# Performance work log

Hardware: AMD Instinct MI355X
Metric: run time of the kernel (lower is better)

## Reference

```python
import jax, jax.numpy as jnp
import numpy as np

DIM = 512; QS = 64; QT = 16; KS = 256; KT = 16; WIN = 4; B = 8; RANK = 32


def build_local_mask():
    # centers = round(linspace(0, kv_steps-1, q_steps)); valid kv step iff |s - center| <= window
    centers = np.round(np.linspace(0.0, KS - 1, QS)).astype(np.int64)
    s = np.arange(KS)
    valid = np.abs(s[None, :] - centers[:, None]) <= WIN  # [QS, KS]
    m = np.where(valid, 0.0, -np.inf).astype(np.float32)
    m = np.repeat(np.repeat(m, QT, axis=0), KT, axis=1)  # [QS*QT, KS*KT]
    return jnp.asarray(m)


def layer_norm(x, g, b, eps=1e-5):
    mu = jnp.mean(x, axis=-1, keepdims=True)
    var = jnp.mean((x - mu) ** 2, axis=-1, keepdims=True)
    return (x - mu) * jax.lax.rsqrt(var + eps) * g + b


def setup_inputs() -> dict:
    key = jax.random.key(0)
    ks = jax.random.split(key, 16)
    w = lambda k, shape: (jax.random.normal(k, shape, jnp.float32) * 0.02)
    return {
        'query': jax.random.normal(ks[0], (B, QS, QT, DIM), jnp.float32),
        'source': jax.random.normal(ks[1], (B, KS, KT, DIM), jnp.float32),
        'ctx0': jax.random.normal(ks[2], (B, DIM), jnp.float32),
        'ctx1': jax.random.normal(ks[3], (B, DIM), jnp.float32),
        'mask': build_local_mask(),
        'qn_g': jnp.ones(DIM), 'qn_b': jnp.zeros(DIM),
        'kvn_g': jnp.ones(DIM), 'kvn_b': jnp.zeros(DIM),
        'Wq': w(ks[4], (DIM, DIM)), 'bq': jnp.zeros(DIM),
        'Wk': w(ks[5], (DIM, DIM)), 'bk': jnp.zeros(DIM),
        'Wv': w(ks[6], (DIM, DIM)), 'bv': jnp.zeros(DIM),
        'Wo': w(ks[7], (DIM, DIM)), 'bo': jnp.zeros(DIM),
        'Wgq': w(ks[8], (DIM, RANK)),
        'Wgk': w(ks[9], (DIM, RANK)),
        'Wc0': w(ks[10], (DIM, DIM)), 'bc0': jnp.zeros(DIM),
        'Wc1': w(ks[11], (DIM, DIM)), 'bc1': jnp.zeros(DIM),
        'Wf': w(ks[12], (DIM, 2 * DIM)), 'bf': jnp.zeros(2 * DIM),
    }


def reference(query, source, ctx0, ctx1, mask, qn_g, qn_b, kvn_g, kvn_b,
              Wq, bq, Wk, bk, Wv, bv, Wo, bo, Wgq, Wgk,
              Wc0, bc0, Wc1, bc1, Wf, bf):
    b = query.shape[0]
    # MultiContextCondition: per-context linear, pooled, FiLM head -> (gamma, beta)
    h = jax.nn.silu(ctx0 @ Wc0 + bc0 + ctx1 @ Wc1 + bc1)          # [b, dim]
    gamma, beta = jnp.split(h @ Wf + bf, 2, axis=-1)              # [b, dim] each
    q_flat = query.reshape(b, QS * QT, DIM)
    s_flat = source.reshape(b, KS * KT, DIM)
    q_base = layer_norm(q_flat, qn_g, qn_b)
    s_base = layer_norm(s_flat, kvn_g, kvn_b)
    q_mod = q_base * (1.0 + gamma[:, None, :]) + beta[:, None, :]
    q_p = q_mod @ Wq + bq
    k_p = s_base @ Wk + bk
    v_p = s_base @ Wv + bv
    scale = DIM ** -0.5
    scores = jnp.einsum('bqd,bkd->bqk', q_p, k_p) * scale          # [b, 1024, 4096]
    gate_q = q_p @ Wgq                                            # [b, q, rank]
    gate_k = k_p @ Wgk                                            # [b, k, rank]
    gate_logits = jnp.einsum('bqr,bkr->bqk', gate_q, gate_k) / np.float32(np.sqrt(RANK))
    gate_bias = jnp.log(jax.nn.sigmoid(gate_logits) + 1e-6)
    scores = scores + mask[None, :, :] + gate_bias
    attn = jax.nn.softmax(scores, axis=-1)
    out = jnp.einsum('bqk,bkd->bqd', attn, v_p) @ Wo + bo
    return out.reshape(b, QS, QT, DIM)
```

## Files before the change

kernel.cpp:

```cpp
#include <hip/hip_runtime.h>
#include <math.h>

#define DIMD 512
#define QS 64
#define KS 256
#define WIN 4
#define BATCH 8
#define RANK 32
#define NQ 1024
#define NK 4096
#define MQ (BATCH*NQ)
#define MK (BATCH*NK)

typedef unsigned short u16;
typedef __attribute__((ext_vector_type(8))) short bf16x8;
typedef __attribute__((ext_vector_type(4))) float f32x4;

__device__ inline u16 f2bf(float x) {
    union { float f; unsigned int u; } v; v.f = x;
    unsigned int r = v.u + 0x7FFF + ((v.u >> 16) & 1);
    return (u16)(r >> 16);
}
__device__ inline float bf2f(u16 x) {
    union { unsigned int u; float f; } v; v.u = ((unsigned int)x) << 16;
    return v.f;
}

__device__ __forceinline__ void gload16(const u16* g, u16* l) {
    __builtin_amdgcn_global_load_lds(
        (const __attribute__((address_space(1))) void*)g,
        (__attribute__((address_space(3))) void*)l, 16, 0, 0);
}


__device__ __forceinline__ void stage_row(const float* src, int r, float* ldsw, int lane) {
    const float* s_ = src + r * DIMD + lane * 4;
    float* d_ = ldsw + (r & 3) * 512;
    gload16((const u16*)s_, (u16*)(d_ + lane * 4));
    gload16((const u16*)(s_ + 256), (u16*)(d_ + 256 + lane * 4));
}

#define WAITV(n) asm volatile("s_waitcnt vmcnt(" #n ")" ::: "memory")

template<bool WRITE_OUT>
__device__ __forceinline__ void norm_staged16(
    int widx, const float* __restrict__ X, const float* __restrict__ g,
    const float* __restrict__ bb, u16* __restrict__ out,
    float* __restrict__ mu_o, float* __restrict__ rs_o, float* ldsw)
{
    int lane = threadIdx.x & 63;
    long row0 = (long)widx * 16;

    float4 g0, g1, b0, b1;
    if (WRITE_OUT) {
        g0 = *(const float4*)&g[lane * 4];
        g1 = *(const float4*)&g[256 + lane * 4];
        b0 = *(const float4*)&bb[lane * 4];
        b1 = *(const float4*)&bb[256 + lane * 4];
    }
    WAITV(0);
    __builtin_amdgcn_sched_barrier(0);

    const float* src = X + row0 * DIMD;

    stage_row(src, 0, ldsw, lane);
    stage_row(src, 1, ldsw, lane);
    stage_row(src, 2, ldsw, lane);
    stage_row(src, 3, ldsw, lane);

    #pragma unroll
    for (int r = 0; r < 16; r++) {
        if (r == 0 || r == 15)      WAITV(6);
        else if (r == 1 || r == 14) WAITV(8);
        else if (r == 2 || r == 13) WAITV(10);
        else                        WAITV(12);
        __builtin_amdgcn_sched_barrier(0);

        const float* rowp = ldsw + (r & 3) * 512;
        float4 a = *(const float4*)&rowp[lane * 4];
        float4 b = *(const float4*)&rowp[256 + lane * 4];

        float s = a.x + a.y + a.z + a.w + b.x + b.y + b.z + b.w;
        float q = a.x*a.x + a.y*a.y + a.z*a.z + a.w*a.w
                + b.x*b.x + b.y*b.y + b.z*b.z + b.w*b.w;
        #pragma unroll
        for (int o = 1; o < 64; o <<= 1) {
            s += __shfl_xor(s, o);
            q += __shfl_xor(q, o);
        }
        float mu = s * (1.f / DIMD);
        float rs = rsqrtf(q * (1.f / DIMD) - mu * mu + 1e-5f);

        if (WRITE_OUT) {
            u16 o4[4];
            o4[0] = f2bf((a.x - mu) * rs * g0.x + b0.x);
            o4[1] = f2bf((a.y - mu) * rs * g0.y + b0.y);
            o4[2] = f2bf((a.z - mu) * rs * g0.z + b0.z);
            o4[3] = f2bf((a.w - mu) * rs * g0.w + b0.w);
            *(int2*)&out[(row0 + r) * DIMD + lane * 4] = *(const int2*)o4;
            o4[0] = f2bf((b.x - mu) * rs * g1.x + b1.x);
            o4[1] = f2bf((b.y - mu) * rs * g1.y + b1.y);
            o4[2] = f2bf((b.z - mu) * rs * g1.z + b1.z);
            o4[3] = f2bf((b.w - mu) * rs * g1.w + b1.w);
            *(int2*)&out[(row0 + r) * DIMD + 256 + lane * 4] = *(const int2*)o4;
        } else {
            if (lane == 0) {
                mu_o[row0 + r] = mu;
                rs_o[row0 + r] = rs;
            }
        }
        if (r + 4 < 16) stage_row(src, r + 4, ldsw, lane);
    }
}

__device__ __forceinline__ void film_h16(
    int bid, const float* __restrict__ ctx0, const float* __restrict__ ctx1,
    const float* __restrict__ Wc0, const float* __restrict__ bc0,
    const float* __restrict__ Wc1, const float* __restrict__ bc1,
    float* __restrict__ h)
{
    int b = bid >> 5;
    int d0 = (bid & 31) * 16;
    int t = threadIdx.x;
    int p = t & 15, dl = t >> 4;
    int d = d0 + dl;
    const float* c0 = ctx0 + b * DIMD;
    const float* c1 = ctx1 + b * DIMD;
    float acc = 0.f;
    #pragma unroll 8
    for (int ii = 0; ii < 32; ii++) {
        int i = p * 32 + ii;
        acc = fmaf(c0[i], Wc0[i * DIMD + d], acc);
        acc = fmaf(c1[i], Wc1[i * DIMD + d], acc);
    }
    acc += __shfl_xor(acc, 1);
    acc += __shfl_xor(acc, 2);
    acc += __shfl_xor(acc, 4);
    acc += __shfl_xor(acc, 8);
    if (p == 0) {
        float v = acc + bc0[d] + bc1[d];
        h[b * DIMD + d] = v / (1.f + expf(-v));
    }
}

__device__ __forceinline__ void film_gb16(
    int bid, const float* __restrict__ h, const float* __restrict__ Wf,
    const float* __restrict__ bfv, float* __restrict__ gamma, float* __restrict__ beta)
{
    int b = bid >> 5;
    int d0 = (bid & 31) * 16;
    int t = threadIdx.x;
    int p = t & 15, dl = t >> 4;
    int d = d0 + dl;
    const float* hb = h + b * DIMD;
    float ga = 0.f, be = 0.f;
    #pragma unroll 8
    for (int ii = 0; ii < 32; ii++) {
        int i = p * 32 + ii;
        float hv = hb[i];
        ga = fmaf(hv, Wf[i * 2 * DIMD + d], ga);
        be = fmaf(hv, Wf[i * 2 * DIMD + DIMD + d], be);
    }
    #pragma unroll
    for (int o = 1; o < 16; o <<= 1) {
        ga += __shfl_xor(ga, o);
        be += __shfl_xor(be, o);
// ... 44 lines not shown
    int cid, const float* __restrict__ b0, const float* __restrict__ b1,
    const float* __restrict__ Wg, float* __restrict__ dst)
{
    int tid = threadIdx.x;
    if (cid < 4) {
        int t = cid * 256 + tid;
        if (t < 512) dst[t] = b0[t];
        else dst[t] = b1[t - 512];
    } else {
        int r = tid >> 3, sp = tid & 7;
        float a = 0.f;
        #pragma unroll 8
        for (int jj = 0; jj < 64; jj++) {
            int j = sp * 64 + jj;
            a = fmaf(b0[j], Wg[j * RANK + r], a);
        }
        a += __shfl_xor(a, 1);
        a += __shfl_xor(a, 2);
        a += __shfl_xor(a, 4);
        if (sp == 0) dst[1024 + r] = a;
    }
}

__device__ __forceinline__ void biascat2_body(
    int cid, const float* __restrict__ b0, const float* __restrict__ Wg,
    float* __restrict__ dst)
{
    int tid = threadIdx.x;
    if (cid < 2) {
        int t = cid * 256 + tid;
        dst[t] = b0[t];
    } else {
        int r = tid >> 3, sp = tid & 7;
        float a = 0.f;
        #pragma unroll 8
        for (int jj = 0; jj < 64; jj++) {
            int j = sp * 64 + jj;
            a = fmaf(b0[j], Wg[j * RANK + r], a);
        }
        a += __shfl_xor(a, 1);
        a += __shfl_xor(a, 2);
        a += __shfl_xor(a, 4);
        if (sp == 0) dst[512 + r] = a;
    }
}

template<int NSEC, bool BF>
__device__ __forceinline__ void gemm_body(
    int id, const u16* __restrict__ A, const u16* __restrict__ Bt,
    const float* __restrict__ biascat,
    void* __restrict__ C0v, void* __restrict__ C1v, void* __restrict__ Cgv,
    int Nvalid, int nx, int ypg, u16* smem)
{
    u16* As = smem;
    u16* Bs = smem + 8192;

    int t = threadIdx.x;
    int wave = t >> 6, lane = t & 63;
    int xcd = id & 7, li = id >> 3;
    int by = xcd * ypg + li / nx;
    int bx = li % nx;
    int m0 = by * 128, n0 = bx * 128;
    int mhalf = (wave >> 1) * 64, nhalf = (wave & 1) * 64;
    int lm = lane & 15, quad = lane >> 4;

    int srow = wave * 8 + (lane >> 3);
    int scol = ((lane & 7) ^ (lane >> 3)) * 8;
    const u16* Ag = A + (long)(m0 + srow) * DIMD + scol;
    const u16* Bg = Bt + (long)(n0 + srow) * DIMD + scol;
    u16* Asl = As + wave * 512 + lane * 8;
    u16* Bsl = Bs + wave * 512 + lane * 8;

    f32x4 acc[4][4];
    #pragma unroll
    for (int i = 0; i < 4; i++)
        #pragma unroll
        for (int j = 0; j < 4; j++)
            acc[i][j] = (f32x4){0.f, 0.f, 0.f, 0.f};

    for (int k0 = 0; k0 < DIMD; k0 += 64) {
        __syncthreads();
        #pragma unroll
        for (int g = 0; g < 4; g++) {
            gload16(Ag + k0 + g * 32 * DIMD, Asl + g * 2048);
            gload16(Bg + k0 + g * 32 * DIMD, Bsl + g * 2048);
        }
        __syncthreads();
        #pragma unroll
        for (int kk = 0; kk < 2; kk++) {
            bf16x8 af[4], bfr[4];
            #pragma unroll
            for (int i = 0; i < 4; i++) {
                int pc = ((kk * 4 + quad) ^ (lm & 7)) << 3;
                af[i]  = *(const bf16x8*)&As[(mhalf + i * 16 + lm) * 64 + pc];
                bfr[i] = *(const bf16x8*)&Bs[(nhalf + i * 16 + lm) * 64 + pc];
            }
            #pragma unroll
            for (int i = 0; i < 4; i++)
                #pragma unroll
                for (int j = 0; j < 4; j++)
                    acc[i][j] = __builtin_amdgcn_mfma_f32_16x16x32_bf16(af[i], bfr[j], acc[i][j], 0, 0, 0);
        }
    }

    float biasj[4];
    #pragma unroll
    for (int j = 0; j < 4; j++) biasj[j] = biascat[n0 + nhalf + j * 16 + lm];

    if (BF) {
        #pragma unroll
        for (int p = 0; p < 2; p++) {
            __syncthreads();
            #pragma unroll
            for (int ii = 0; ii < 2; ii++) {
                int i = p * 2 + ii;
                #pragma unroll
                for (int j = 0; j < 4; j++)
                    #pragma unroll
                    for (int r = 0; r < 4; r++)
                        smem[(ii * 32 + (wave >> 1) * 16 + quad * 4 + r) * 136 + nhalf + j * 16 + lm] =
                            f2bf(acc[i][j][r] + biasj[j]);
            }
            __syncthreads();
            #pragma unroll
            for (int u = 0; u < 4; u++) {
                int cch = t + u * 256;
                int R = cch >> 4, ci = cch & 15;
                int i = p * 2 + (R >> 5);
                int Rr = R & 31;
                long grow = m0 + (Rr >> 4) * 64 + i * 16 + (Rr & 15);
                int gcol = n0 + ci * 8;
                int4 val = *(const int4*)&smem[R * 136 + ci * 8];
                if (NSEC == 1) {
                    *(int4*)((u16*)C0v + grow * 512 + gcol) = val;
                } else if (NSEC == 2) {
                    if (gcol < 512)          *(int4*)((u16*)C0v + grow * 512 + gcol) = val;
                    else if (gcol < Nvalid)  *(int4*)((u16*)Cgv + grow * 32 + (gcol - 512)) = val;
                } else {
                    if (gcol < 512)          *(int4*)((u16*)C0v + grow * 512 + gcol) = val;
                    else if (gcol < 1024)    *(int4*)((u16*)C1v + grow * 512 + (gcol - 512)) = val;
                    else if (gcol < Nvalid)  *(int4*)((u16*)Cgv + grow * 32 + (gcol - 1024)) = val;
                }
            }
        }
    } else {
        float* Stg = (float*)smem;
        for (int i = 0; i < 4; i++) {
            __syncthreads();
            #pragma unroll
            for (int j = 0; j < 4; j++)
                #pragma unroll
                for (int r = 0; r < 4; r++)
                    Stg[((wave >> 1) * 16 + quad * 4 + r) * 132 + nhalf + j * 16 + lm] =
                        acc[i][j][r] + biasj[j];
            __syncthreads();
            #pragma unroll
            for (int u = 0; u < 4; u++) {
                int cch = t + u * 256;
                int R = cch >> 5, ci = cch & 31;
                long grow = m0 + (R >> 4) * 64 + i * 16 + (R & 15);
                int gcol = n0 + ci * 4;
                *(float4*)((float*)C0v + grow * 512 + gcol) = *(const float4*)&Stg[R * 132 + ci * 4];
            }
        }
    }
}

#define PREP_FILMH   256
#define PREP_GATE    (PREP_FILMH + 512)
#define PREP_BIAS    (PREP_GATE + 8)
#define PREP_TRANS   (PREP_BIAS + 1024)
#define PREP_STATS   (PREP_TRANS + 128)
#define PREP_TOTAL   (PREP_STATS + 512)

__global__ __launch_bounds__(256) void prep_kernel(
    const float* __restrict__ source, const float* __restrict__ kvn_g,
    const float* __restrict__ kvn_b, u16* __restrict__ sln,
    const float* __restrict__ query, float* __restrict__ mu_q, float* __restrict__ rs_q,
    const float* __restrict__ ctx0, const float* __restrict__ ctx1,
    const float* __restrict__ Wc0, const float* __restrict__ bc0,
    const float* __restrict__ Wc1, const float* __restrict__ bc1,
    float* __restrict__ h,
    const float* __restrict__ Wk, const float* __restrict__ Wv,
    const float* __restrict__ Wq, const float* __restrict__ Wo,
    u16* __restrict__ Btkv, u16* __restrict__ Btq, u16* __restrict__ Bto,
    const float* __restrict__ Wgk, const float* __restrict__ Wgq,
    const float* __restrict__ bk, const float* __restrict__ bv,
    const float* __restrict__ bq, float* __restrict__ biaskv,
    float* __restrict__ biasq)
{
    __shared__ float tile[32][33];
    __shared__ float stg[4][2048];
    int bid = blockIdx.x;
    int wave = threadIdx.x >> 6;
    if (bid < PREP_FILMH) {
        film_h16(bid, ctx0, ctx1, Wc0, bc0, Wc1, bc1, h);
    } else if (bid < PREP_GATE) {
        int gid = bid - PREP_FILMH;
        if (gid < 256) gatefuse4(gid, Wk, Wgk, Btkv, 1024);
        else           gatefuse4(gid, Wq, Wgq, Btq, 512);
    } else if (bid < PREP_BIAS) {
        int cid = bid - PREP_GATE;
        if (cid < 5) biascat3_body(cid, bk, bv, Wgk, biaskv);
        else         biascat2_body(cid - 5, bq, Wgq, biasq);
    } else if (bid < PREP_TRANS) {
        int tid = bid - PREP_BIAS;
        int which = tid >> 8, i = tid & 255;
        if (which == 0)      transpose_body(i, Wk, Btkv, 0, tile);
        else if (which == 1) transpose_body(i, Wv, Btkv, 512, tile);
        else if (which == 2) transpose_body(i, Wq, Btq, 0, tile);
        else                 transpose_body(i, Wo, Bto, 0, tile);
    } else if (bid < PREP_STATS) {
        norm_staged16<false>((bid - PREP_TRANS) * 4 + wave, query,
                             nullptr, nullptr, nullptr, mu_q, rs_q, stg[wave]);
    } else {
        norm_staged16<true>((bid - PREP_STATS) * 4 + wave, source,
                            kvn_g, kvn_b, sln, nullptr, nullptr, stg[wave]);
    }
}

__global__ __launch_bounds__(256) void kv_kernel(
    const float* __restrict__ h, const float* __restrict__ Wf,
    const float* __restrict__ bfv, float* __restrict__ gamma, float* __restrict__ beta,
    const u16* __restrict__ sln, const u16* __restrict__ Btkv,
    const float* __restrict__ biaskv,
    u16* __restrict__ kp, u16* __restrict__ vp, u16* __restrict__ gk)
{
    __shared__ u16 smem[16384];
    int bid = blockIdx.x;
    if (bid < 256) {
        film_gb16(bid, h, Wf, bfv, gamma, beta);
    } else {
        gemm_body<3, true>(bid - 256, sln, Btkv, biaskv, kp, vp, gk, 1056, 9, 32, smem);
    }
}

__global__ __launch_bounds__(256) void qproj_kernel(
    const float* __restrict__ query, const float* __restrict__ mu_q,
    const float* __restrict__ rs_q, const float* __restrict__ qn_g,
    const float* __restrict__ qn_b, const float* __restrict__ gamma,
    const float* __restrict__ beta, const u16* __restrict__ Btq,
    const float* __restrict__ biasq, u16* __restrict__ qp, u16* __restrict__ gq)
{
    __shared__ u16 smem[8192];
    u16* As = smem;
    u16* Bs = smem + 4096;

    int t = threadIdx.x;
    int wave = t >> 6, lane = t & 63;
    int id = blockIdx.x;
    int xcd = id & 7, li = id >> 3;
    int by = xcd * 8 + li / 5;
    int bx = li % 5;
    int m0 = by * 128, n0 = bx * 128;
    int mhalf = (wave >> 1) * 64, nhalf = (wave & 1) * 64;
    int lm = lane & 15, quad = lane >> 4;
    int bt = m0 >> 10;

    int srow = wave * 32 + (lane >> 2);
    int scol = (lane & 3) * 8;
    const u16* Bg = Btq + (long)(n0 + srow) * DIMD + scol;
    u16* Bsl = Bs + wave * 1024 + lane * 8;

    f32x4 acc[4][4];
    #pragma unroll
    for (int i = 0; i < 4; i++)
        #pragma unroll
        for (int j = 0; j < 4; j++)
            acc[i][j] = (f32x4){0.f, 0.f, 0.f, 0.f};

    for (int k0 = 0; k0 < DIMD; k0 += 32) {
        __syncthreads();
        gload16(Bg + k0, Bsl);
        gload16(Bg + 16 * DIMD + k0, Bsl + 512);
        #pragma unroll
        for (int u = 0; u < 2; u++) {
            int idx = t + u * 256;
            int r = idx >> 2;
            int c8 = (idx & 3) * 8;
            long grow = m0 + r;
            int col = k0 + c8;
            const float* xp = &query[grow * DIMD + col];
            float4 x0 = *(const float4*)xp, x1 = *(const float4*)(xp + 4);
            float mu = mu_q[grow], rs = rs_q[grow];
            float4 g0 = *(const float4*)&qn_g[col], g1 = *(const float4*)&qn_g[col + 4];
            float4 b0 = *(const float4*)&qn_b[col], b1 = *(const float4*)&qn_b[col + 4];
// ... 6 lines not shown
            o8[1] = f2bf(((x0.y - mu) * rs * g0.y + b0.y) * (1.f + gm0.y) + be0.y);
            o8[2] = f2bf(((x0.z - mu) * rs * g0.z + b0.z) * (1.f + gm0.z) + be0.z);
            o8[3] = f2bf(((x0.w - mu) * rs * g0.w + b0.w) * (1.f + gm0.w) + be0.w);
            o8[4] = f2bf(((x1.x - mu) * rs * g1.x + b1.x) * (1.f + gm1.x) + be1.x);
            o8[5] = f2bf(((x1.y - mu) * rs * g1.y + b1.y) * (1.f + gm1.y) + be1.y);
            o8[6] = f2bf(((x1.z - mu) * rs * g1.z + b1.z) * (1.f + gm1.z) + be1.z);
            o8[7] = f2bf(((x1.w - mu) * rs * g1.w + b1.w) * (1.f + gm1.w) + be1.w);
            *(int4*)&As[r * 32 + c8] = *(const int4*)o8;
        }
        __syncthreads();
        bf16x8 af[4], bfr[4];
        #pragma unroll
        for (int i = 0; i < 4; i++) {
            af[i]  = *(const bf16x8*)&As[(mhalf + i * 16 + lm) * 32 + quad * 8];
            bfr[i] = *(const bf16x8*)&Bs[(nhalf + i * 16 + lm) * 32 + quad * 8];
        }
        #pragma unroll
        for (int i = 0; i < 4; i++)
            #pragma unroll
            for (int j = 0; j < 4; j++)
                acc[i][j] = __builtin_amdgcn_mfma_f32_16x16x32_bf16(af[i], bfr[j], acc[i][j], 0, 0, 0);
    }

    float biasj[4];
    #pragma unroll
    for (int j = 0; j < 4; j++) biasj[j] = biasq[n0 + nhalf + j * 16 + lm];

    for (int i = 0; i < 4; i++) {
        __syncthreads();
        #pragma unroll
        for (int j = 0; j < 4; j++)
            #pragma unroll
            for (int r = 0; r < 4; r++)
                smem[((wave >> 1) * 16 + quad * 4 + r) * 128 + nhalf + j * 16 + lm] =
                    f2bf(acc[i][j][r] + biasj[j]);
        __syncthreads();
        #pragma unroll
        for (int u = 0; u < 2; u++) {
            int cch = t + u * 256;
            int R = cch >> 4, ci = cch & 15;
            long grow = m0 + (R >> 4) * 64 + i * 16 + (R & 15);
            int gcol = n0 + ci * 8;
            int4 val = *(const int4*)&smem[R * 128 + ci * 8];
            if (gcol < 512)       *(int4*)(qp + grow * 512 + gcol) = val;
            else if (gcol < 544)  *(int4*)(gq + grow * 32 + (gcol - 512)) = val;
        }
    }
}

__global__ __launch_bounds__(256) void ogemm_kernel(
    const u16* __restrict__ ctxb, const u16* __restrict__ Bto,
    const float* __restrict__ bo, float* __restrict__ out)
{
    __shared__ u16 smem[16384];
    gemm_body<1, false>(blockIdx.x, ctxb, Bto, bo, out, nullptr, nullptr, 512, 4, 8, smem);
}

__global__ __launch_bounds__(256, 2) void attn_kernel(
    const u16* __restrict__ q_bf, const u16* __restrict__ k_bf,
    const u16* __restrict__ v_bf, const u16* __restrict__ gq_bf,
    const u16* __restrict__ gk_bf, u16* __restrict__ ctx)
{
    __shared__ u16 Ks[16 * 512];
    __shared__ u16 Vt[512 * 32];
    __shared__ u16 Pb[16 * 40];
    __shared__ float part[4][16][16];
    __shared__ float Gb[16][16];
    __shared__ float alphap[16];
    __shared__ float linv[16];

    int blk = blockIdx.x;
    int b = blk >> 6, qs = blk & 63;
    int center = (int)(qs * (255.0f / 63.0f) + 0.5f);
    int lo = center - WIN; if (lo < 0) lo = 0;
    int hi = center + WIN; if (hi > KS - 1) hi = KS - 1;
    int nst = hi - lo + 1;
    long rowq0 = (long)b * NQ + qs * 16;
    long rowk0 = (long)b * NK + lo * 16;

    int t = threadIdx.x;
    int wave = t >> 6, lane = t & 63;
    int lm = lane & 15, quad = lane >> 4;
    int qi = t >> 4, ki = t & 15;

    bf16x8 qf[4];
    #pragma unroll
    for (int f = 0; f < 4; f++)
        qf[f] = *(const bf16x8*)&q_bf[(rowq0 + lm) * DIMD + wave * 128 + f * 32 + quad * 8];
    bf16x8 gqf;
    if (wave == 3) gqf = *(const bf16x8*)&gq_bf[(rowq0 + lm) * RANK + quad * 8];

    int4 kpre[4], vpre[4];
    #pragma unroll
    for (int u = 0; u < 4; u++) {
        int idx = u * 256 + t;
        kpre[u] = *(const int4*)&k_bf[(rowk0 + (idx >> 6)) * DIMD + (idx & 63) * 8];
        int vkv = (idx >> 2) & 15, vdc = (idx & 3) | ((idx >> 6) << 2);
        vpre[u] = *(const int4*)&v_bf[(rowk0 + vkv) * DIMD + vdc * 8];
    }

    float m_run = -1e30f, l_run = 0.f;
    f32x4 acc[8];
    #pragma unroll
    for (int j = 0; j < 8; j++) acc[j] = (f32x4){0.f, 0.f, 0.f, 0.f};

    const float scale = 0.044194173824159216f;
    const float grs = 0.17677669529663687f;
// ... 83 lines not shown
                #pragma unroll
                for (int r = 0; r < 4; r++) acc[j][r] *= ar[r];
            bf16x8 pf = *(const bf16x8*)&Pb[lm * 40 + quad * 8];
            #pragma unroll
            for (int j = 0; j < 8; j++) {
                int d = wave * 128 + j * 16 + lm;
                bf16x8 vf = *(const bf16x8*)&Vt[d * 32 + ((quad ^ (d & 3)) << 3)];
                acc[j] = __builtin_amdgcn_mfma_f32_16x16x32_bf16(pf, vf, acc[j], 0, 0, 0);
            }
            __syncthreads();
        }
    }
    float li[4];
    #pragma unroll
    for (int r = 0; r < 4; r++) li[r] = linv[quad * 4 + r];
    #pragma unroll
    for (int j = 0; j < 8; j++) {
        int d = wave * 128 + j * 16 + lm;
        #pragma unroll
        for (int r = 0; r < 4; r++)
            ctx[(rowq0 + quad * 4 + r) * DIMD + d] = f2bf(acc[j][r] * li[r]);
    }
}

extern "C" void kernel_launch(void* const* d_in, const int* in_sizes, int n_in,
                              void* d_out, int out_size, void* d_ws, size_t ws_size,
                              hipStream_t stream) {
    const float* query  = (const float*)d_in[0];
    const float* source = (const float*)d_in[1];
    const float* ctx0   = (const float*)d_in[2];
    const float* ctx1   = (const float*)d_in[3];
    const float* qn_g  = (const float*)d_in[5];
    const float* qn_b  = (const float*)d_in[6];
    const float* kvn_g = (const float*)d_in[7];
    const float* kvn_b = (const float*)d_in[8];
    const float* Wq = (const float*)d_in[9];   const float* bq = (const float*)d_in[10];
    const float* Wk = (const float*)d_in[11];  const float* bk = (const float*)d_in[12];
    const float* Wv = (const float*)d_in[13];  const float* bv = (const float*)d_in[14];
    const float* Wo = (const float*)d_in[15];  const float* bo = (const float*)d_in[16];
    const float* Wgq = (const float*)d_in[17];
    const float* Wgk = (const float*)d_in[18];
    const float* Wc0 = (const float*)d_in[19]; const float* bc0 = (const float*)d_in[20];
    const float* Wc1 = (const float*)d_in[21]; const float* bc1 = (const float*)d_in[22];
    const float* Wf  = (const float*)d_in[23]; const float* bfv = (const float*)d_in[24];

    float* ws = (float*)d_ws;
    float* h      = ws;
    float* gamma  = h + 4096;
    float* beta   = gamma + 4096;
    float* biaskv = beta + 4096;
    float* biasq  = biaskv + 1152;
    float* mu_q   = biasq + 640;
    float* rs_q   = mu_q + 8192;
    u16* u = (u16*)(rs_q + 8192);
    u16* sln  = u;                 u += (long)MK * DIMD;
    u16* kp   = u;                 u += (long)MK * DIMD;
    u16* vp   = u;                 u += (long)MK * DIMD;
    u16* gk   = u;                 u += (long)MK * RANK;
    u16* gq   = u;                 u += (long)MQ * RANK;
    u16* qp   = u;                 u += (long)MQ * DIMD;
    u16* ctxb = u;                 u += (long)MQ * DIMD;
    u16* Btkv = u;                 u += 1152L * DIMD;
    u16* Btq  = u;                 u += 640L * DIMD;
    u16* Bto  = u;                 u += 512L * DIMD;
    float* out = (float*)d_out;

    prep_kernel<<<PREP_TOTAL, 256, 0, stream>>>(
        source, kvn_g, kvn_b, sln,
        query, mu_q, rs_q,
        ctx0, ctx1, Wc0, bc0, Wc1, bc1, h,
        Wk, Wv, Wq, Wo, Btkv, Btq, Bto,
        Wgk, Wgq, bk, bv, bq, biaskv, biasq);

    kv_kernel<<<256 + 2304, 256, 0, stream>>>(
        h, Wf, bfv, gamma, beta, sln, Btkv, biaskv, kp, vp, gk);

    qproj_kernel<<<320, 256, 0, stream>>>(
        query, mu_q, rs_q, qn_g, qn_b, gamma, beta, Btq, biasq, qp, gq);

    attn_kernel<<<BATCH * QS, 256, 0, stream>>>(qp, kp, vp, gq, gk, ctxb);

    ogemm_kernel<<<256, 256, 0, stream>>>(ctxb, Bto, bo, out);
}
```

Before: 361.2 us.

## Fuse source layernorm into KV projection GEMM using precomputed row stats

The source layernorm no longer writes a bf16 normalized copy (sln). A stats-only pass now computes per-row mean and rstd, and the KV GEMM reads fp32 source directly, normalizing and converting to bf16 while staging the A tile into LDS. This removes the write and re-read of a 32K x 512 bf16 intermediate. In exchange the GEMM reads fp32 source, which is twice the bytes of the bf16 copy, and each source tile is read once per N-tile column block (9 times). The prep kernel is also split into a weight kernel and a stats kernel, adding one extra launch.

Measured after the change: 392.1 us. 8.5% more time.

```diff
diff --git a/kernel.cpp b/kernel.cpp
--- a/kernel.cpp
+++ b/kernel.cpp
@@ -42,22 +42,13 @@
 
 #define WAITV(n) asm volatile("s_waitcnt vmcnt(" #n ")" ::: "memory")
 
-template<bool WRITE_OUT>
-__device__ __forceinline__ void norm_staged16(
-    int widx, const float* __restrict__ X, const float* __restrict__ g,
-    const float* __restrict__ bb, u16* __restrict__ out,
+__device__ __forceinline__ void stats_staged16(
+    int widx, const float* __restrict__ X,
     float* __restrict__ mu_o, float* __restrict__ rs_o, float* ldsw)
 {
     int lane = threadIdx.x & 63;
     long row0 = (long)widx * 16;
 
-    float4 g0, g1, b0, b1;
-    if (WRITE_OUT) {
-        g0 = *(const float4*)&g[lane * 4];
-        g1 = *(const float4*)&g[256 + lane * 4];
-        b0 = *(const float4*)&bb[lane * 4];
-        b1 = *(const float4*)&bb[256 + lane * 4];
-    }
     WAITV(0);
     __builtin_amdgcn_sched_barrier(0);
 
@@ -70,10 +61,11 @@
 
     #pragma unroll
     for (int r = 0; r < 16; r++) {
-        if (r == 0 || r == 15)      WAITV(6);
-        else if (r == 1 || r == 14) WAITV(8);
-        else if (r == 2 || r == 13) WAITV(10);
-        else                        WAITV(12);
+        if (r < 12)      WAITV(6);
+        else if (r == 12) WAITV(6);
+        else if (r == 13) WAITV(4);
+        else if (r == 14) WAITV(2);
+        else              WAITV(0);
         __builtin_amdgcn_sched_barrier(0);
 
         const float* rowp = ldsw + (r & 3) * 512;
@@ -88,26 +80,10 @@
             s += __shfl_xor(s, o);
             q += __shfl_xor(q, o);
         }
-        float mu = s * (1.f / DIMD);
-        float rs = rsqrtf(q * (1.f / DIMD) - mu * mu + 1e-5f);
-
-        if (WRITE_OUT) {
-            u16 o4[4];
-            o4[0] = f2bf((a.x - mu) * rs * g0.x + b0.x);
-            o4[1] = f2bf((a.y - mu) * rs * g0.y + b0.y);
-            o4[2] = f2bf((a.z - mu) * rs * g0.z + b0.z);
-            o4[3] = f2bf((a.w - mu) * rs * g0.w + b0.w);
-            *(int2*)&out[(row0 + r) * DIMD + lane * 4] = *(const int2*)o4;
-            o4[0] = f2bf((b.x - mu) * rs * g1.x + b1.x);
-            o4[1] = f2bf((b.y - mu) * rs * g1.y + b1.y);
-            o4[2] = f2bf((b.z - mu) * rs * g1.z + b1.z);
-            o4[3] = f2bf((b.w - mu) * rs * g1.w + b1.w);
-            *(int2*)&out[(row0 + r) * DIMD + 256 + lane * 4] = *(const int2*)o4;
-        } else {
-            if (lane == 0) {
-                mu_o[row0 + r] = mu;
-                rs_o[row0 + r] = rs;
-            }
+        if (lane == 0) {
+            float mu = s * (1.f / DIMD);
+            mu_o[row0 + r] = mu;
+            rs_o[row0 + r] = rsqrtf(q * (1.f / DIMD) - mu * mu + 1e-5f);
         }
         if (r + 4 < 16) stage_row(src, r + 4, ldsw, lane);
     }
@@ -376,17 +352,12 @@
     }
 }
 
-#define PREP_FILMH   256
-#define PREP_GATE    (PREP_FILMH + 512)
-#define PREP_BIAS    (PREP_GATE + 8)
-#define PREP_TRANS   (PREP_BIAS + 1024)
-#define PREP_STATS   (PREP_TRANS + 128)
-#define PREP_TOTAL   (PREP_STATS + 512)
-
-__global__ __launch_bounds__(256) void prep_kernel(
-    const float* __restrict__ source, const float* __restrict__ kvn_g,
-    const float* __restrict__ kvn_b, u16* __restrict__ sln,
-    const float* __restrict__ query, float* __restrict__ mu_q, float* __restrict__ rs_q,
+#define PW_FILMH   256
+#define PW_GATE    (PW_FILMH + 512)
+#define PW_BIAS    (PW_GATE + 8)
+#define PW_TOTAL   (PW_BIAS + 1024)
+
+__global__ __launch_bounds__(256) void prep_w_kernel(
     const float* __restrict__ ctx0, const float* __restrict__ ctx1,
     const float* __restrict__ Wc0, const float* __restrict__ bc0,
     const float* __restrict__ Wc1, const float* __restrict__ bc1,
@@ -400,39 +371,50 @@
     float* __restrict__ biasq)
 {
     __shared__ float tile[32][33];
-    __shared__ float stg[4][2048];
     int bid = blockIdx.x;
-    int wave = threadIdx.x >> 6;
-    if (bid < PREP_FILMH) {
+    if (bid < PW_FILMH) {
         film_h16(bid, ctx0, ctx1, Wc0, bc0, Wc1, bc1, h);
-    } else if (bid < PREP_GATE) {
-        int gid = bid - PREP_FILMH;
+    } else if (bid < PW_GATE) {
+        int gid = bid - PW_FILMH;
         if (gid < 256) gatefuse4(gid, Wk, Wgk, Btkv, 1024);
         else           gatefuse4(gid, Wq, Wgq, Btq, 512);
-    } else if (bid < PREP_BIAS) {
-        int cid = bid - PREP_GATE;
+    } else if (bid < PW_BIAS) {
+        int cid = bid - PW_GATE;
         if (cid < 5) biascat3_body(cid, bk, bv, Wgk, biaskv);
         else         biascat2_body(cid - 5, bq, Wgq, biasq);
-    } else if (bid < PREP_TRANS) {
-        int tid = bid - PREP_BIAS;
+    } else {
+        int tid = bid - PW_BIAS;
         int which = tid >> 8, i = tid & 255;
         if (which == 0)      transpose_body(i, Wk, Btkv, 0, tile);
         else if (which == 1) transpose_body(i, Wv, Btkv, 512, tile);
         else if (which == 2) transpose_body(i, Wq, Btq, 0, tile);
         else                 transpose_body(i, Wo, Bto, 0, tile);
-    } else if (bid < PREP_STATS) {
-        norm_staged16<false>((bid - PREP_TRANS) * 4 + wave, query,
-                             nullptr, nullptr, nullptr, mu_q, rs_q, stg[wave]);
+    }
+}
+
+#define PS_QSTAT   128
+#define PS_TOTAL   (PS_QSTAT + 512)
+
+__global__ __launch_bounds__(256) void prep_s_kernel(
+    const float* __restrict__ query, float* __restrict__ mu_q, float* __restrict__ rs_q,
+    const float* __restrict__ source, float* __restrict__ mu_s, float* __restrict__ rs_s)
+{
+    __shared__ float stg[4][2048];
+    int bid = blockIdx.x;
+    int wave = threadIdx.x >> 6;
+    if (bid < PS_QSTAT) {
+        stats_staged16(bid * 4 + wave, query, mu_q, rs_q, stg[wave]);
     } else {
-        norm_staged16<true>((bid - PREP_STATS) * 4 + wave, source,
-                            kvn_g, kvn_b, sln, nullptr, nullptr, stg[wave]);
+        stats_staged16((bid - PS_QSTAT) * 4 + wave, source, mu_s, rs_s, stg[wave]);
     }
 }
 
 __global__ __launch_bounds__(256) void kv_kernel(
     const float* __restrict__ h, const float* __restrict__ Wf,
     const float* __restrict__ bfv, float* __restrict__ gamma, float* __restrict__ beta,
-    const u16* __restrict__ sln, const u16* __restrict__ Btkv,
+    const float* __restrict__ source, const float* __restrict__ mu_s,
+    const float* __restrict__ rs_s, const float* __restrict__ kvn_g,
+    const float* __restrict__ kvn_b, const u16* __restrict__ Btkv,
     const float* __restrict__ biaskv,
     u16* __restrict__ kp, u16* __restrict__ vp, u16* __restrict__ gk)
 {
@@ -440,8 +422,111 @@
     int bid = blockIdx.x;
     if (bid < 256) {
         film_gb16(bid, h, Wf, bfv, gamma, beta);
-    } else {
-        gemm_body<3, true>(bid - 256, sln, Btkv, biaskv, kp, vp, gk, 1056, 9, 32, smem);
+        return;
+    }
+    u16* As = smem;
+    u16* Bs = smem + 8192;
+
+    int t = threadIdx.x;
+    int wave = t >> 6, lane = t & 63;
+    int id = bid - 256;
+    int xcd = id & 7, li = id >> 3;
+    int by = xcd * 32 + li / 9;
+    int bx = li % 9;
+    int m0 = by * 128, n0 = bx * 128;
+    int mhalf = (wave >> 1) * 64, nhalf = (wave & 1) * 64;
+    int lm = lane & 15, quad = lane >> 4;
+
+    int srow = wave * 8 + (lane >> 3);
+    int scol = ((lane & 7) ^ (lane >> 3)) * 8;
+    const u16* Bg = Btkv + (long)(n0 + srow) * DIMD + scol;
+    u16* Bsl = Bs + wave * 512 + lane * 8;
+
+    f32x4 acc[4][4];
+    #pragma unroll
+    for (int i = 0; i < 4; i++)
+        #pragma unroll
+        for (int j = 0; j < 4; j++)
+            acc[i][j] = (f32x4){0.f, 0.f, 0.f, 0.f};
+
+    for (int k0 = 0; k0 < DIMD; k0 += 64) {
+        __syncthreads();
+        #pragma unroll
+        for (int g = 0; g < 4; g++)
+            gload16(Bg + k0 + g * 32 * DIMD, Bsl + g * 2048);
+        #pragma unroll
+        for (int u = 0; u < 4; u++) {
+            int idx = t + u * 256;
+            int r = idx >> 3;
+            int c8 = (idx & 7) * 8;
+            long grow = m0 + r;
+            int col = k0 + c8;
+            const float* xp = &source[grow * DIMD + col];
+            float4 x0 = *(const float4*)xp, x1 = *(const float4*)(xp + 4);
+            float mu = mu_s[grow], rs = rs_s[grow];
+            float4 g0 = *(const float4*)&kvn_g[col], g1 = *(const float4*)&kvn_g[col + 4];
+            float4 b0 = *(const float4*)&kvn_b[col], b1 = *(const float4*)&kvn_b[col + 4];
+            u16 o8[8];
+            o8[0] = f2bf((x0.x - mu) * rs * g0.x + b0.x);
+            o8[1] = f2bf((x0.y - mu) * rs * g0.y + b0.y);
+            o8[2] = f2bf((x0.z - mu) * rs * g0.z + b0.z);
+            o8[3] = f2bf((x0.w - mu) * rs * g0.w + b0.w);
+            o8[4] = f2bf((x1.x - mu) * rs * g1.x + b1.x);
+            o8[5] = f2bf((x1.y - mu) * rs * g1.y + b1.y);
+            o8[6] = f2bf((x1.z - mu) * rs * g1.z + b1.z);
+            o8[7] = f2bf((x1.w - mu) * rs * g1.w + b1.w);
+            int pc = ((c8 >> 3) ^ (r & 7)) << 3;
+            *(int4*)&As[r * 64 + pc] = *(const int4*)o8;
+        }
+        __syncthreads();
+        #pragma unroll
+        for (int kk = 0; kk < 2; kk++) {
+            bf16x8 af[4], bfr[4];
+            #pragma unroll
+            for (int i = 0; i < 4; i++) {
+                int pc = ((kk * 4 + quad) ^ (lm & 7)) << 3;
+                af[i]  = *(const bf16x8*)&As[(mhalf + i * 16 + lm) * 64 + pc];
+                bfr[i] = *(const bf16x8*)&Bs[(nhalf + i * 16 + lm) * 64 + pc];
+            }
+            #pragma unroll
+            for (int i = 0; i < 4; i++)
+                #pragma unroll
+                for (int j = 0; j < 4; j++)
+                    acc[i][j] = __builtin_amdgcn_mfma_f32_16x16x32_bf16(af[i], bfr[j], acc[i][j], 0, 0, 0);
+        }
+    }
+
+    float biasj[4];
+    #pragma unroll
+    for (int j = 0; j < 4; j++) biasj[j] = biaskv[n0 + nhalf + j * 16 + lm];
+
+    #pragma unroll
+    for (int p = 0; p < 2; p++) {
+        __syncthreads();
+        #pragma unroll
+        for (int ii = 0; ii < 2; ii++) {
+            int i = p * 2 + ii;
+            #pragma unroll
+            for (int j = 0; j < 4; j++)
+                #pragma unroll
+                for (int r = 0; r < 4; r++)
+                    smem[(ii * 32 + (wave >> 1) * 16 + quad * 4 + r) * 136 + nhalf + j * 16 + lm] =
+                        f2bf(acc[i][j][r] + biasj[j]);
+        }
+        __syncthreads();
+        #pragma unroll
+        for (int u = 0; u < 4; u++) {
+            int cch = t + u * 256;
+            int R = cch >> 4, ci = cch & 15;
+            int i = p * 2 + (R >> 5);
+            int Rr = R & 31;
+            long grow = m0 + (Rr >> 4) * 64 + i * 16 + (Rr & 15);
+            int gcol = n0 + ci * 8;
+            int4 val = *(const int4*)&smem[R * 136 + ci * 8];
+            if (gcol < 512)          *(int4*)(kp + grow * 512 + gcol) = val;
+            else if (gcol < 1024)    *(int4*)(vp + grow * 512 + (gcol - 512)) = val;
+            else if (gcol < 1056)    *(int4*)(gk + grow * 32 + (gcol - 1024)) = val;
+        }
     }
 }
 
@@ -744,8 +829,9 @@
     float* biasq  = biaskv + 1152;
     float* mu_q   = biasq + 640;
     float* rs_q   = mu_q + 8192;
-    u16* u = (u16*)(rs_q + 8192);
-    u16* sln  = u;                 u += (long)MK * DIMD;
+    float* mu_s   = rs_q + 8192;
+    float* rs_s   = mu_s + 32768;
+    u16* u = (u16*)(rs_s + 32768);
     u16* kp   = u;                 u += (long)MK * DIMD;
     u16* vp   = u;                 u += (long)MK * DIMD;
     u16* gk   = u;                 u += (long)MK * RANK;
@@ -757,15 +843,18 @@
     u16* Bto  = u;                 u += 512L * DIMD;
     float* out = (float*)d_out;
 
-    prep_kernel<<<PREP_TOTAL, 256, 0, stream>>>(
-        source, kvn_g, kvn_b, sln,
-        query, mu_q, rs_q,
+    prep_w_kernel<<<PW_TOTAL, 256, 0, stream>>>(
         ctx0, ctx1, Wc0, bc0, Wc1, bc1, h,
         Wk, Wv, Wq, Wo, Btkv, Btq, Bto,
         Wgk, Wgq, bk, bv, bq, biaskv, biasq);
 
+    prep_s_kernel<<<PS_TOTAL, 256, 0, stream>>>(
+        query, mu_q, rs_q, source, mu_s, rs_s);
+
     kv_kernel<<<256 + 2304, 256, 0, stream>>>(
-        h, Wf, bfv, gamma, beta, sln, Btkv, biaskv, kp, vp, gk);
+        h, Wf, bfv, gamma, beta,
+        source, mu_s, rs_s, kvn_g, kvn_b,
+        Btkv, biaskv, kp, vp, gk);
 
     qproj_kernel<<<320, 256, 0, stream>>>(
         query, mu_q, rs_q, qn_g, qn_b, gamma, beta, Btq, biasq, qp, gq);
```

## Replace LDS-staged layernorm with direct loads and LDS row-sum reduction

Applied to the files above, without the earlier changes.

The layernorm/stats path drops the global_load_lds staging pipeline with manual vmcnt waits. Each lane now loads 8 contiguous floats per row straight into registers and writes per-lane partial sums to LDS. The partials are reduced across 16 rows at once, which replaces the per-row 6-step shuffle reduction. The normalize pass re-reads the source rows from global memory and writes 16-byte bf16 stores, trading a second read of the input for fewer shuffles and wider stores.

Result: no change. 367.5 us (+1.8%).

```diff
diff --git a/kernel.cpp b/kernel.cpp
--- a/kernel.cpp
+++ b/kernel.cpp
@@ -33,83 +33,84 @@
 }
 
 
-__device__ __forceinline__ void stage_row(const float* src, int r, float* ldsw, int lane) {
-    const float* s_ = src + r * DIMD + lane * 4;
-    float* d_ = ldsw + (r & 3) * 512;
-    gload16((const u16*)s_, (u16*)(d_ + lane * 4));
-    gload16((const u16*)(s_ + 256), (u16*)(d_ + 256 + lane * 4));
-}
-
-#define WAITV(n) asm volatile("s_waitcnt vmcnt(" #n ")" ::: "memory")
-
 template<bool WRITE_OUT>
-__device__ __forceinline__ void norm_staged16(
+__device__ __forceinline__ void stream16(
     int widx, const float* __restrict__ X, const float* __restrict__ g,
     const float* __restrict__ bb, u16* __restrict__ out,
-    float* __restrict__ mu_o, float* __restrict__ rs_o, float* ldsw)
+    float* __restrict__ mu_o, float* __restrict__ rs_o, float* red)
 {
     int lane = threadIdx.x & 63;
     long row0 = (long)widx * 16;
+    const float* src = X + row0 * DIMD;
+    float* ps   = red;
+    float* pq   = red + 16 * 68;
+    float* murs = red + 2 * 16 * 68;
 
     float4 g0, g1, b0, b1;
     if (WRITE_OUT) {
-        g0 = *(const float4*)&g[lane * 4];
-        g1 = *(const float4*)&g[256 + lane * 4];
-        b0 = *(const float4*)&bb[lane * 4];
-        b1 = *(const float4*)&bb[256 + lane * 4];
-    }
-    WAITV(0);
-    __builtin_amdgcn_sched_barrier(0);
-
-    const float* src = X + row0 * DIMD;
-
-    stage_row(src, 0, ldsw, lane);
-    stage_row(src, 1, ldsw, lane);
-    stage_row(src, 2, ldsw, lane);
-    stage_row(src, 3, ldsw, lane);
+        g0 = *(const float4*)&g[lane * 8];
+        g1 = *(const float4*)&g[lane * 8 + 4];
+        b0 = *(const float4*)&bb[lane * 8];
+        b1 = *(const float4*)&bb[lane * 8 + 4];
+    }
 
     #pragma unroll
     for (int r = 0; r < 16; r++) {
-        if (r == 0 || r == 15)      WAITV(6);
-        else if (r == 1 || r == 14) WAITV(8);
-        else if (r == 2 || r == 13) WAITV(10);
-        else                        WAITV(12);
-        __builtin_amdgcn_sched_barrier(0);
-
-        const float* rowp = ldsw + (r & 3) * 512;
-        float4 a = *(const float4*)&rowp[lane * 4];
-        float4 b = *(const float4*)&rowp[256 + lane * 4];
-
+        const float* xp = src + r * DIMD + lane * 8;
+        float4 a = *(const float4*)xp;
+        float4 b = *(const float4*)(xp + 4);
         float s = a.x + a.y + a.z + a.w + b.x + b.y + b.z + b.w;
         float q = a.x*a.x + a.y*a.y + a.z*a.z + a.w*a.w
                 + b.x*b.x + b.y*b.y + b.z*b.z + b.w*b.w;
-        #pragma unroll
-        for (int o = 1; o < 64; o <<= 1) {
-            s += __shfl_xor(s, o);
-            q += __shfl_xor(q, o);
-        }
-        float mu = s * (1.f / DIMD);
-        float rs = rsqrtf(q * (1.f / DIMD) - mu * mu + 1e-5f);
-
-        if (WRITE_OUT) {
-            u16 o4[4];
-            o4[0] = f2bf((a.x - mu) * rs * g0.x + b0.x);
-            o4[1] = f2bf((a.y - mu) * rs * g0.y + b0.y);
-            o4[2] = f2bf((a.z - mu) * rs * g0.z + b0.z);
-            o4[3] = f2bf((a.w - mu) * rs * g0.w + b0.w);
-            *(int2*)&out[(row0 + r) * DIMD + lane * 4] = *(const int2*)o4;
-            o4[0] = f2bf((b.x - mu) * rs * g1.x + b1.x);
-            o4[1] = f2bf((b.y - mu) * rs * g1.y + b1.y);
-            o4[2] = f2bf((b.z - mu) * rs * g1.z + b1.z);
-            o4[3] = f2bf((b.w - mu) * rs * g1.w + b1.w);
-            *(int2*)&out[(row0 + r) * DIMD + 256 + lane * 4] = *(const int2*)o4;
-        } else {
-            if (lane == 0) {
-                mu_o[row0 + r] = mu;
-                rs_o[row0 + r] = rs;
+        ps[r * 68 + lane] = s;
+        pq[r * 68 + lane] = q;
+    }
+    __syncthreads();
+
+    {
+        int row = lane & 15, qtr = lane >> 4;
+        float ss = 0.f, qq = 0.f;
+        #pragma unroll
+        for (int j = 0; j < 16; j += 4) {
+            float4 v = *(const float4*)&ps[row * 68 + qtr * 16 + j];
+            ss += v.x + v.y + v.z + v.w;
+            float4 w = *(const float4*)&pq[row * 68 + qtr * 16 + j];
+            qq += w.x + w.y + w.z + w.w;
+        }
+        ss += __shfl_xor(ss, 16); ss += __shfl_xor(ss, 32);
+        qq += __shfl_xor(qq, 16); qq += __shfl_xor(qq, 32);
+        if (qtr == 0) {
+            float mu = ss * (1.f / DIMD);
+            float rs = rsqrtf(qq * (1.f / DIMD) - mu * mu + 1e-5f);
+            if (WRITE_OUT) {
+                murs[row] = mu;
+                murs[16 + row] = rs;
+            } else {
+                mu_o[row0 + row] = mu;
+                rs_o[row0 + row] = rs;
             }
         }
-        if (r + 4 < 16) stage_row(src, r + 4, ldsw, lane);
+    }
+
+    if (WRITE_OUT) {
+        __syncthreads();
+        #pragma unroll
+        for (int r = 0; r < 16; r++) {
+            float mu = murs[r], rs = murs[16 + r];
+            const float* xp = src + r * DIMD + lane * 8;
+            float4 a = *(const float4*)xp;
+            float4 b = *(const float4*)(xp + 4);
+            u16 o8[8];
+            o8[0] = f2bf((a.x - mu) * rs * g0.x + b0.x);
+            o8[1] = f2bf((a.y - mu) * rs * g0.y + b0.y);
+            o8[2] = f2bf((a.z - mu) * rs * g0.z + b0.z);
+            o8[3] = f2bf((a.w - mu) * rs * g0.w + b0.w);
+            o8[4] = f2bf((b.x - mu) * rs * g1.x + b1.x);
+            o8[5] = f2bf((b.y - mu) * rs * g1.y + b1.y);
+            o8[6] = f2bf((b.z - mu) * rs * g1.z + b1.z);
+            o8[7] = f2bf((b.w - mu) * rs * g1.w + b1.w);
+            *(int4*)&out[(row0 + r) * DIMD + lane * 8] = *(const int4*)o8;
+        }
     }
 }
 
@@ -400,7 +401,7 @@
     float* __restrict__ biasq)
 {
     __shared__ float tile[32][33];
-    __shared__ float stg[4][2048];
+    __shared__ float sred[4][2 * 16 * 68 + 32];
     int bid = blockIdx.x;
     int wave = threadIdx.x >> 6;
     if (bid < PREP_FILMH) {
@@ -421,11 +422,11 @@
         else if (which == 2) transpose_body(i, Wq, Btq, 0, tile);
         else                 transpose_body(i, Wo, Bto, 0, tile);
     } else if (bid < PREP_STATS) {
-        norm_staged16<false>((bid - PREP_TRANS) * 4 + wave, query,
-                             nullptr, nullptr, nullptr, mu_q, rs_q, stg[wave]);
+        stream16<false>((bid - PREP_TRANS) * 4 + wave, query,
+                        nullptr, nullptr, nullptr, mu_q, rs_q, sred[wave]);
     } else {
-        norm_staged16<true>((bid - PREP_STATS) * 4 + wave, source,
-                            kvn_g, kvn_b, sln, nullptr, nullptr, stg[wave]);
+        stream16<true>((bid - PREP_STATS) * 4 + wave, source,
+                       kvn_g, kvn_b, sln, nullptr, nullptr, sred[wave]);
     }
 }
 
```

## Double-buffer GEMM LDS tiles and split layernorm prep into grid-stride kernel

Applied to the files above, without the earlier changes.

The shared GEMM body now double-buffers its A/B tiles in LDS, prefetching the next k-slice with async global-to-LDS loads while MFMAs run on the current one. This hides load latency and halves the barriers per iteration, but doubles LDS to 64KB per block, which may reduce occupancy. Separately, the monolithic prep kernel is split into a weight-prep kernel and a grid-stride layernorm kernel. The new kernel replaces the LDS-staged 16-row-per-wave pipeline with direct vectorized loads of 8 floats per lane and 16-byte stores.

Measured after the change: 352.6 us. -2.4%, faster.

```diff
diff --git a/kernel.cpp b/kernel.cpp
--- a/kernel.cpp
+++ b/kernel.cpp
@@ -32,86 +32,8 @@
         (__attribute__((address_space(3))) void*)l, 16, 0, 0);
 }
 
-
-__device__ __forceinline__ void stage_row(const float* src, int r, float* ldsw, int lane) {
-    const float* s_ = src + r * DIMD + lane * 4;
-    float* d_ = ldsw + (r & 3) * 512;
-    gload16((const u16*)s_, (u16*)(d_ + lane * 4));
-    gload16((const u16*)(s_ + 256), (u16*)(d_ + 256 + lane * 4));
-}
-
 #define WAITV(n) asm volatile("s_waitcnt vmcnt(" #n ")" ::: "memory")
 
-template<bool WRITE_OUT>
-__device__ __forceinline__ void norm_staged16(
-    int widx, const float* __restrict__ X, const float* __restrict__ g,
-    const float* __restrict__ bb, u16* __restrict__ out,
-    float* __restrict__ mu_o, float* __restrict__ rs_o, float* ldsw)
-{
-    int lane = threadIdx.x & 63;
-    long row0 = (long)widx * 16;
-
-    float4 g0, g1, b0, b1;
-    if (WRITE_OUT) {
-        g0 = *(const float4*)&g[lane * 4];
-        g1 = *(const float4*)&g[256 + lane * 4];
-        b0 = *(const float4*)&bb[lane * 4];
-        b1 = *(const float4*)&bb[256 + lane * 4];
-    }
-    WAITV(0);
-    __builtin_amdgcn_sched_barrier(0);
-
-    const float* src = X + row0 * DIMD;
-
-    stage_row(src, 0, ldsw, lane);
-    stage_row(src, 1, ldsw, lane);
-    stage_row(src, 2, ldsw, lane);
-    stage_row(src, 3, ldsw, lane);
-
-    #pragma unroll
-    for (int r = 0; r < 16; r++) {
-        if (r == 0 || r == 15)      WAITV(6);
-        else if (r == 1 || r == 14) WAITV(8);
-        else if (r == 2 || r == 13) WAITV(10);
-        else                        WAITV(12);
-        __builtin_amdgcn_sched_barrier(0);
-
-        const float* rowp = ldsw + (r & 3) * 512;
-        float4 a = *(const float4*)&rowp[lane * 4];
-        float4 b = *(const float4*)&rowp[256 + lane * 4];
-
-        float s = a.x + a.y + a.z + a.w + b.x + b.y + b.z + b.w;
-        float q = a.x*a.x + a.y*a.y + a.z*a.z + a.w*a.w
-                + b.x*b.x + b.y*b.y + b.z*b.z + b.w*b.w;
-        #pragma unroll
-        for (int o = 1; o < 64; o <<= 1) {
-            s += __shfl_xor(s, o);
-            q += __shfl_xor(q, o);
-        }
-        float mu = s * (1.f / DIMD);
-        float rs = rsqrtf(q * (1.f / DIMD) - mu * mu + 1e-5f);
-
-        if (WRITE_OUT) {
-            u16 o4[4];
-            o4[0] = f2bf((a.x - mu) * rs * g0.x + b0.x);
-            o4[1] = f2bf((a.y - mu) * rs * g0.y + b0.y);
-            o4[2] = f2bf((a.z - mu) * rs * g0.z + b0.z);
-            o4[3] = f2bf((a.w - mu) * rs * g0.w + b0.w);
-            *(int2*)&out[(row0 + r) * DIMD + lane * 4] = *(const int2*)o4;
-            o4[0] = f2bf((b.x - mu) * rs * g1.x + b1.x);
-            o4[1] = f2bf((b.y - mu) * rs * g1.y + b1.y);
-            o4[2] = f2bf((b.z - mu) * rs * g1.z + b1.z);
-            o4[3] = f2bf((b.w - mu) * rs * g1.w + b1.w);
-            *(int2*)&out[(row0 + r) * DIMD + 256 + lane * 4] = *(const int2*)o4;
-        } else {
-            if (lane == 0) {
-                mu_o[row0 + r] = mu;
-                rs_o[row0 + r] = rs;
-            }
-        }
-        if (r + 4 < 16) stage_row(src, r + 4, ldsw, lane);
-    }
-}
 
 __device__ __forceinline__ void film_h16(
     int bid, const float* __restrict__ ctx0, const float* __restrict__ ctx1,
@@ -262,9 +184,6 @@
     void* __restrict__ C0v, void* __restrict__ C1v, void* __restrict__ Cgv,
     int Nvalid, int nx, int ypg, u16* smem)
 {
-    u16* As = smem;
-    u16* Bs = smem + 8192;
-
     int t = threadIdx.x;
     int wave = t >> 6, lane = t & 63;
     int xcd = id & 7, li = id >> 3;
@@ -278,8 +197,7 @@
     int scol = ((lane & 7) ^ (lane >> 3)) * 8;
     const u16* Ag = A + (long)(m0 + srow) * DIMD + scol;
     const u16* Bg = Bt + (long)(n0 + srow) * DIMD + scol;
-    u16* Asl = As + wave * 512 + lane * 8;
-    u16* Bsl = Bs + wave * 512 + lane * 8;
+    int loff = wave * 512 + lane * 8;
 
     f32x4 acc[4][4];
     #pragma unroll
@@ -288,14 +206,27 @@
         for (int j = 0; j < 4; j++)
             acc[i][j] = (f32x4){0.f, 0.f, 0.f, 0.f};
 
+    #pragma unroll
+    for (int g = 0; g < 4; g++) {
+        gload16(Ag + g * 32 * DIMD, smem + loff + g * 2048);
+        gload16(Bg + g * 32 * DIMD, smem + 8192 + loff + g * 2048);
+    }
+    WAITV(0);
+    __syncthreads();
+
+    int cur = 0;
     for (int k0 = 0; k0 < DIMD; k0 += 64) {
-        __syncthreads();
-        #pragma unroll
-        for (int g = 0; g < 4; g++) {
-            gload16(Ag + k0 + g * 32 * DIMD, Asl + g * 2048);
-            gload16(Bg + k0 + g * 32 * DIMD, Bsl + g * 2048);
-        }
-        __syncthreads();
+        if (k0 + 64 < DIMD) {
+            u16* Asl = smem + (cur ^ 1) * 16384 + loff;
+            u16* Bsl = smem + (cur ^ 1) * 16384 + 8192 + loff;
+            #pragma unroll
+            for (int g = 0; g < 4; g++) {
+                gload16(Ag + k0 + 64 + g * 32 * DIMD, Asl + g * 2048);
+                gload16(Bg + k0 + 64 + g * 32 * DIMD, Bsl + g * 2048);
+            }
+        }
+        const u16* As = smem + cur * 16384;
+        const u16* Bs = smem + cur * 16384 + 8192;
         #pragma unroll
         for (int kk = 0; kk < 2; kk++) {
             bf16x8 af[4], bfr[4];
@@ -311,6 +242,9 @@
                 for (int j = 0; j < 4; j++)
                     acc[i][j] = __builtin_amdgcn_mfma_f32_16x16x32_bf16(af[i], bfr[j], acc[i][j], 0, 0, 0);
         }
+        WAITV(0);
+        __syncthreads();
+        cur ^= 1;
     }
 
     float biasj[4];
@@ -376,17 +310,12 @@
     }
 }
 
-#define PREP_FILMH   256
-#define PREP_GATE    (PREP_FILMH + 512)
-#define PREP_BIAS    (PREP_GATE + 8)
-#define PREP_TRANS   (PREP_BIAS + 1024)
-#define PREP_STATS   (PREP_TRANS + 128)
-#define PREP_TOTAL   (PREP_STATS + 512)
-
-__global__ __launch_bounds__(256) void prep_kernel(
-    const float* __restrict__ source, const float* __restrict__ kvn_g,
-    const float* __restrict__ kvn_b, u16* __restrict__ sln,
-    const float* __restrict__ query, float* __restrict__ mu_q, float* __restrict__ rs_q,
+#define PW_FILMH   256
+#define PW_GATE    (PW_FILMH + 512)
+#define PW_BIAS    (PW_GATE + 8)
+#define PW_TOTAL   (PW_BIAS + 1024)
+
+__global__ __launch_bounds__(256) void prep_w_kernel(
     const float* __restrict__ ctx0, const float* __restrict__ ctx1,
     const float* __restrict__ Wc0, const float* __restrict__ bc0,
     const float* __restrict__ Wc1, const float* __restrict__ bc1,
@@ -400,32 +329,73 @@
     float* __restrict__ biasq)
 {
     __shared__ float tile[32][33];
-    __shared__ float stg[4][2048];
     int bid = blockIdx.x;
-    int wave = threadIdx.x >> 6;
-    if (bid < PREP_FILMH) {
+    if (bid < PW_FILMH) {
         film_h16(bid, ctx0, ctx1, Wc0, bc0, Wc1, bc1, h);
-    } else if (bid < PREP_GATE) {
-        int gid = bid - PREP_FILMH;
+    } else if (bid < PW_GATE) {
+        int gid = bid - PW_FILMH;
         if (gid < 256) gatefuse4(gid, Wk, Wgk, Btkv, 1024);
         else           gatefuse4(gid, Wq, Wgq, Btq, 512);
-    } else if (bid < PREP_BIAS) {
-        int cid = bid - PREP_GATE;
+    } else if (bid < PW_BIAS) {
+        int cid = bid - PW_GATE;
         if (cid < 5) biascat3_body(cid, bk, bv, Wgk, biaskv);
         else         biascat2_body(cid - 5, bq, Wgq, biasq);
-    } else if (bid < PREP_TRANS) {
-        int tid = bid - PREP_BIAS;
+    } else {
+        int tid = bid - PW_BIAS;
         int which = tid >> 8, i = tid & 255;
         if (which == 0)      transpose_body(i, Wk, Btkv, 0, tile);
         else if (which == 1) transpose_body(i, Wv, Btkv, 512, tile);
         else if (which == 2) transpose_body(i, Wq, Btq, 0, tile);
         else                 transpose_body(i, Wo, Bto, 0, tile);
-    } else if (bid < PREP_STATS) {
-        norm_staged16<false>((bid - PREP_TRANS) * 4 + wave, query,
-                             nullptr, nullptr, nullptr, mu_q, rs_q, stg[wave]);
-    } else {
-        norm_staged16<true>((bid - PREP_STATS) * 4 + wave, source,
-                            kvn_g, kvn_b, sln, nullptr, nullptr, stg[wave]);
+    }
+}
+
+#define PS_BLOCKS 2048
+
+__global__ __launch_bounds__(256) void prep_s_kernel(
+    const float* __restrict__ query, float* __restrict__ mu_q, float* __restrict__ rs_q,
+    const float* __restrict__ source, const float* __restrict__ kvn_g,
+    const float* __restrict__ kvn_b, u16* __restrict__ sln)
+{
+    int lane = threadIdx.x & 63;
+    int gw = blockIdx.x * 4 + (threadIdx.x >> 6);
+    int c = lane * 8;
+    float4 g0 = *(const float4*)&kvn_g[c], g1 = *(const float4*)&kvn_g[c + 4];
+    float4 b0 = *(const float4*)&kvn_b[c], b1 = *(const float4*)&kvn_b[c + 4];
+
+    for (long row = gw; row < (long)(MQ + MK); row += PS_BLOCKS * 4) {
+        const float* x = (row < MQ)
+            ? query + row * DIMD + c
+            : source + (row - MQ) * DIMD + c;
+        float4 a = *(const float4*)x;
+        float4 b = *(const float4*)(x + 4);
+        float s = a.x + a.y + a.z + a.w + b.x + b.y + b.z + b.w;
+        float q = a.x*a.x + a.y*a.y + a.z*a.z + a.w*a.w
+                + b.x*b.x + b.y*b.y + b.z*b.z + b.w*b.w;
+        #pragma unroll
+        for (int o = 1; o < 64; o <<= 1) {
+            s += __shfl_xor(s, o);
+            q += __shfl_xor(q, o);
+        }
+        float mu = s * (1.f / DIMD);
+        float rs = rsqrtf(q * (1.f / DIMD) - mu * mu + 1e-5f);
+        if (row < MQ) {
+            if (lane == 0) {
+                mu_q[row] = mu;
+                rs_q[row] = rs;
+            }
+        } else {
+            u16 o8[8];
+            o8[0] = f2bf((a.x - mu) * rs * g0.x + b0.x);
+            o8[1] = f2bf((a.y - mu) * rs * g0.y + b0.y);
+            o8[2] = f2bf((a.z - mu) * rs * g0.z + b0.z);
+            o8[3] = f2bf((a.w - mu) * rs * g0.w + b0.w);
+            o8[4] = f2bf((b.x - mu) * rs * g1.x + b1.x);
+            o8[5] = f2bf((b.y - mu) * rs * g1.y + b1.y);
+            o8[6] = f2bf((b.z - mu) * rs * g1.z + b1.z);
+            o8[7] = f2bf((b.w - mu) * rs * g1.w + b1.w);
+            *(int4*)&sln[(row - MQ) * DIMD + c] = *(const int4*)o8;
+        }
     }
 }
 
@@ -436,7 +406,7 @@
     const float* __restrict__ biaskv,
     u16* __restrict__ kp, u16* __restrict__ vp, u16* __restrict__ gk)
 {
-    __shared__ u16 smem[16384];
+    __shared__ u16 smem[32768];
     int bid = blockIdx.x;
     if (bid < 256) {
         film_gb16(bid, h, Wf, bfv, gamma, beta);
@@ -554,7 +524,7 @@
     const u16* __restrict__ ctxb, const u16* __restrict__ Bto,
     const float* __restrict__ bo, float* __restrict__ out)
 {
-    __shared__ u16 smem[16384];
+    __shared__ u16 smem[32768];
     gemm_body<1, false>(blockIdx.x, ctxb, Bto, bo, out, nullptr, nullptr, 512, 4, 8, smem);
 }
 
@@ -757,13 +727,14 @@
     u16* Bto  = u;                 u += 512L * DIMD;
     float* out = (float*)d_out;
 
-    prep_kernel<<<PREP_TOTAL, 256, 0, stream>>>(
-        source, kvn_g, kvn_b, sln,
-        query, mu_q, rs_q,
+    prep_w_kernel<<<PW_TOTAL, 256, 0, stream>>>(
         ctx0, ctx1, Wc0, bc0, Wc1, bc1, h,
         Wk, Wv, Wq, Wo, Btkv, Btq, Bto,
         Wgk, Wgq, bk, bv, bq, biaskv, biasq);
 
+    prep_s_kernel<<<PS_BLOCKS, 256, 0, stream>>>(
+        query, mu_q, rs_q, source, kvn_g, kvn_b, sln);
+
     kv_kernel<<<256 + 2304, 256, 0, stream>>>(
         h, Wf, bfv, gamma, beta, sln, Btkv, biaskv, kp, vp, gk);
 
```
